# Optimization experiments

Measured on AMD Instinct MI355X. Metric: run time of the kernel, lower is better.

Reference implementation:

```python
import jax, jax.numpy as jnp
import numpy as np


def setup_inputs() -> dict:
    key = jax.random.key(0)
    B, N, M, D = 8, 256, 16, 256
    embeddings = jax.random.normal(key, (B, N, M, D), dtype=jnp.float32)
    w = jnp.asarray(10.0, dtype=jnp.float32)
    b = jnp.asarray(-5.0, dtype=jnp.float32)
    return {"embeddings": embeddings, "w": w, "b": b}


def reference(embeddings, w, b):
    # embeddings: [B, N, M, D]
    B, N, M, D = embeddings.shape
    centroids = jnp.mean(embeddings, axis=2)  # [B, N, D]

    # Cross similarities: S[b,j,i,k] = w * <e_{bji}, c_{bk}> + b
    S = w * jnp.einsum('bjid,bkd->bjik', embeddings, centroids) + b  # [B,N,M,N]

    # Own-centroid case (j == k): leave-one-out centroid
    # <e, (M*c_j - e)/(M-1)> = (M*<e,c_j> - ||e||^2) / (M-1)
    dot_own = jnp.einsum('bjid,bjd->bji', embeddings, centroids)     # [B,N,M]
    sq_norm = jnp.sum(embeddings * embeddings, axis=-1)              # [B,N,M]
    S_self = w * (M * dot_own - sq_norm) / (M - 1) + b               # [B,N,M]

    # Place S_self on the k == j diagonal
    eye = jnp.eye(N, dtype=bool)[None, :, None, :]                   # [1,N,1,N]
    S = jnp.where(eye, S_self[..., None], S)

    # loss = sum log sum_k exp(S) - sum_{j==k} S
    loss = jnp.sum(jax.nn.logsumexp(S, axis=-1)) - jnp.sum(S_self)
    return loss
```

## Files before the change

### kernel.cpp

```cpp
#include <hip/hip_runtime.h>

constexpr int B = 8, N = 256, M = 16, D = 256;

typedef short bf16x8 __attribute__((ext_vector_type(8)));
typedef float f32x4 __attribute__((ext_vector_type(4)));

__device__ __forceinline__ unsigned short f2bf(float x) {
  unsigned u = __float_as_uint(x);
  u = (u + 0x7FFFu + ((u >> 16) & 1u)) >> 16;
  return (unsigned short)u;
}
__device__ __forceinline__ uint4 packbf8(const float* f) {
  uint4 u;
  u.x = (unsigned)f2bf(f[0]) | ((unsigned)f2bf(f[1]) << 16);
  u.y = (unsigned)f2bf(f[2]) | ((unsigned)f2bf(f[3]) << 16);
  u.z = (unsigned)f2bf(f[4]) | ((unsigned)f2bf(f[5]) << 16);
  u.w = (unsigned)f2bf(f[6]) | ((unsigned)f2bf(f[7]) << 16);
  return u;
}


__global__ __launch_bounds__(256) void k_cent(const float* __restrict__ e,
                                              uint4* __restrict__ Cbf,
                                              float* __restrict__ out) {
  const int blk = blockIdx.x;
  const int b = blk >> 8, j = blk & 255;
  const int t = threadIdx.x;
  const float* base = e + (size_t)blk * (M * D);

  __shared__ float cbuf[D];
  float cs = 0.f;
#pragma unroll
  for (int i = 0; i < M; ++i) cs += base[i * D + t];
  cbuf[t] = cs * (1.f / 16.f);
  __syncthreads();

  if (t < 32) {
    float cf[8];
#pragma unroll
    for (int x = 0; x < 8; ++x) cf[x] = cbuf[t * 8 + x];
    Cbf[((size_t)(b * 8 + (t >> 2)) * 16 + (j >> 4)) * 64 + (t & 3) * 16 + (j & 15)] =
        packbf8(cf);
  }
  if (blk == 0 && t == 0) out[0] = 0.f;
}

__global__ __launch_bounds__(256) void k_gemm2(const float* __restrict__ e,
                                               const uint4* __restrict__ Cbf,
                                               const float* __restrict__ wp,
                                               const float* __restrict__ bp,
                                               float* __restrict__ out) {
  const int blk = blockIdx.x;
  const int b = blk >> 6, strip = blk & 63;
  const int tid = threadIdx.x;
  const int wid = tid >> 6, lane = tid & 63;

  __shared__ uint4 A_lds[4 * 8 * 64];
  __shared__ float sql[64];
  __shared__ float lmx[2][64];
  __shared__ float lsm[2][64];
  __shared__ float bred[4];

  {
    const int j = strip * 4 + wid;
    const float* base = e + (size_t)(b * 256 + j) * (M * D);
    const int m = lane & 15, q = lane >> 4;
    const float* rp = base + m * D + q * 8;
    float sqp = 0.f;
#pragma unroll
    for (int kc = 0; kc < 8; ++kc) {
      float f[8];
      *(float4*)(f) = *(const float4*)(rp + kc * 32);
      *(float4*)(f + 4) = *(const float4*)(rp + kc * 32 + 4);
      A_lds[(wid * 8 + kc) * 64 + lane] = packbf8(f);
#pragma unroll
      for (int x = 0; x < 8; ++x) sqp = fmaf(f[x], f[x], sqp);
    }
    sqp += __shfl_xor(sqp, 16, 64);
    sqp += __shfl_xor(sqp, 32, 64);
    if (q == 0) sql[wid * 16 + m] = sqp;
  }
  __syncthreads();

  const int h = wid >> 1, c = wid & 1;
  const int q = lane >> 4, cl_ = lane & 15;
  const uint4* Bb = Cbf + (size_t)(b * 128 + c * 8) * 64 + lane;

  f32x4 acc[2][8];
#pragma unroll
  for (int rt = 0; rt < 2; ++rt)
#pragma unroll
    for (int nt = 0; nt < 8; ++nt) acc[rt][nt] = (f32x4)0.f;

#pragma unroll 1
  for (int kc = 0; kc < 8; ++kc) {
    uint4 af0 = A_lds[((h * 2) * 8 + kc) * 64 + lane];
    uint4 af1 = A_lds[((h * 2 + 1) * 8 + kc) * 64 + lane];
    uint4 bfr[8];
#pragma unroll
    for (int nt = 0; nt < 8; ++nt) bfr[nt] = Bb[(kc * 16 + nt) * 64];
    bf16x8 a0 = __builtin_bit_cast(bf16x8, af0);
    bf16x8 a1 = __builtin_bit_cast(bf16x8, af1);
#pragma unroll
    for (int nt = 0; nt < 8; ++nt) {
      bf16x8 bv = __builtin_bit_cast(bf16x8, bfr[nt]);
      acc[0][nt] = __builtin_amdgcn_mfma_f32_16x16x32_bf16(a0, bv, acc[0][nt], 0, 0, 0);
      acc[1][nt] = __builtin_amdgcn_mfma_f32_16x16x32_bf16(a1, bv, acc[1][nt], 0, 0, 0);
    }
  }

  const float w = *wp, bias = *bp;
  float ssum = 0.f;

#pragma unroll
  for (int rt = 0; rt < 2; ++rt) {
    const int jr = strip * 4 + h * 2 + rt;
    const bool own = (c == (jr >> 7)) && (cl_ == (jr & 15));
    const int ntd = (jr >> 4) & 7;
    float sq[4];
    if (own) {
#pragma unroll
      for (int reg = 0; reg < 4; ++reg)
        sq[reg] = sql[(h * 2 + rt) * 16 + q * 4 + reg];
    }
#pragma unroll
    for (int nt = 0; nt < 8; ++nt)
#pragma unroll
      for (int reg = 0; reg < 4; ++reg) {
        const float raw = acc[rt][nt][reg];
        float sv = fmaf(w, raw, bias);
        if (own && nt == ntd) {
          sv = fmaf(w * (1.f / 15.f), 16.f * raw - sq[reg], bias);
          ssum += sv;
        }
        acc[rt][nt][reg] = sv;
      }
#pragma unroll
    for (int reg = 0; reg < 4; ++reg) {
      float mx = acc[rt][0][reg];
#pragma unroll
      for (int nt = 1; nt < 8; ++nt) mx = fmaxf(mx, acc[rt][nt][reg]);
#pragma unroll
      for (int mk = 1; mk < 16; mk <<= 1) mx = fmaxf(mx, __shfl_xor(mx, mk, 64));
      if (cl_ == 0) lmx[c][(h * 2 + rt) * 16 + q * 4 + reg] = mx;
    }
  }
  __syncthreads();

#pragma unroll
  for (int rt = 0; rt < 2; ++rt)
#pragma unroll
    for (int reg = 0; reg < 4; ++reg) {
      const int Rl = (h * 2 + rt) * 16 + q * 4 + reg;
      const float mx = fmaxf(lmx[0][Rl], lmx[1][Rl]);
      float se = 0.f;
#pragma unroll
      for (int nt = 0; nt < 8; ++nt) se += __expf(acc[rt][nt][reg] - mx);
#pragma unroll
      for (int mk = 1; mk < 16; mk <<= 1) se += __shfl_xor(se, mk, 64);
      if (cl_ == 0) lsm[c][Rl] = se;
    }
  __syncthreads();

  float part = -ssum;
  if (c == 0 && cl_ == 0) {
#pragma unroll
    for (int rt = 0; rt < 2; ++rt)
#pragma unroll
      for (int reg = 0; reg < 4; ++reg) {
        const int Rl = (h * 2 + rt) * 16 + q * 4 + reg;
        const float mx = fmaxf(lmx[0][Rl], lmx[1][Rl]);
        part += mx + __logf(lsm[0][Rl] + lsm[1][Rl]);
      }
  }
#pragma unroll
  for (int mk = 1; mk < 64; mk <<= 1) part += __shfl_xor(part, mk, 64);
  if (lane == 0) bred[wid] = part;
  __syncthreads();
  if (tid == 0) atomicAdd(out, bred[0] + bred[1] + bred[2] + bred[3]);
}

extern "C" void kernel_launch(void* const* d_in, const int* in_sizes, int n_in,
                              void* d_out, int out_size, void* d_ws, size_t ws_size,
                              hipStream_t stream) {
  const float* e = (const float*)d_in[0];
  const float* wp = (const float*)d_in[1];
  const float* bp = (const float*)d_in[2];
  float* out = (float*)d_out;
  uint4* Cbf = (uint4*)d_ws;

  k_cent<<<B * N, 256, 0, stream>>>(e, Cbf, out);
  k_gemm2<<<B * 64, 256, 0, stream>>>(e, Cbf, wp, bp, out);
}
```

Before: 99.58 us.

## Halve rows per GEMM block to double grid size and parallelism

The fused GEMM+logsumexp kernel now handles 2 centroid rows per block instead of 4, so the grid doubles from 512 to 1024 blocks. Each wave computes one row tile, and the A-tile load and squared norm are split across two waves, with the two partial norms combined through shared memory. This targets under-occupancy on a 256-CU part and cuts per-wave accumulator registers. The cost is that each block now rereads the full centroid B matrix for half as many rows, which doubles centroid traffic through L2.

New measurement: 102.7 us. 1.03x slower.

```diff
diff --git a/kernel.cpp b/kernel.cpp
--- a/kernel.cpp
+++ b/kernel.cpp
@@ -45,133 +45,122 @@
   if (blk == 0 && t == 0) out[0] = 0.f;
 }
 
-__global__ __launch_bounds__(256) void k_gemm2(const float* __restrict__ e,
+__global__ __launch_bounds__(256) void k_gemm3(const float* __restrict__ e,
                                                const uint4* __restrict__ Cbf,
                                                const float* __restrict__ wp,
                                                const float* __restrict__ bp,
                                                float* __restrict__ out) {
   const int blk = blockIdx.x;
-  const int b = blk >> 6, strip = blk & 63;
+  const int b = blk >> 7, p = blk & 127;
   const int tid = threadIdx.x;
   const int wid = tid >> 6, lane = tid & 63;
+  const int jt = wid >> 1, half = wid & 1;
 
-  __shared__ uint4 A_lds[4 * 8 * 64];
-  __shared__ float sql[64];
-  __shared__ float lmx[2][64];
-  __shared__ float lsm[2][64];
+  __shared__ uint4 A_lds[2 * 8 * 64];
+  __shared__ float sqh[2][2][16];
+  __shared__ float lmx[2][32];
+  __shared__ float lsm[2][32];
   __shared__ float bred[4];
 
   {
-    const int j = strip * 4 + wid;
+    const int j = p * 2 + jt;
     const float* base = e + (size_t)(b * 256 + j) * (M * D);
     const int m = lane & 15, q = lane >> 4;
     const float* rp = base + m * D + q * 8;
     float sqp = 0.f;
 #pragma unroll
-    for (int kc = 0; kc < 8; ++kc) {
+    for (int kk = 0; kk < 4; ++kk) {
+      const int kc = half * 4 + kk;
       float f[8];
       *(float4*)(f) = *(const float4*)(rp + kc * 32);
       *(float4*)(f + 4) = *(const float4*)(rp + kc * 32 + 4);
-      A_lds[(wid * 8 + kc) * 64 + lane] = packbf8(f);
+      A_lds[(jt * 8 + kc) * 64 + lane] = packbf8(f);
 #pragma unroll
       for (int x = 0; x < 8; ++x) sqp = fmaf(f[x], f[x], sqp);
     }
     sqp += __shfl_xor(sqp, 16, 64);
     sqp += __shfl_xor(sqp, 32, 64);
-    if (q == 0) sql[wid * 16 + m] = sqp;
+    if (q == 0) sqh[jt][half][m] = sqp;
   }
   __syncthreads();
 
-  const int h = wid >> 1, c = wid & 1;
+  const int c = half;
   const int q = lane >> 4, cl_ = lane & 15;
   const uint4* Bb = Cbf + (size_t)(b * 128 + c * 8) * 64 + lane;
 
-  f32x4 acc[2][8];
+  f32x4 acc[8];
 #pragma unroll
-  for (int rt = 0; rt < 2; ++rt)
-#pragma unroll
-    for (int nt = 0; nt < 8; ++nt) acc[rt][nt] = (f32x4)0.f;
+  for (int nt = 0; nt < 8; ++nt) acc[nt] = (f32x4)0.f;
 
 #pragma unroll 1
   for (int kc = 0; kc < 8; ++kc) {
-    uint4 af0 = A_lds[((h * 2) * 8 + kc) * 64 + lane];
-    uint4 af1 = A_lds[((h * 2 + 1) * 8 + kc) * 64 + lane];
+    uint4 af = A_lds[(jt * 8 + kc) * 64 + lane];
     uint4 bfr[8];
 #pragma unroll
     for (int nt = 0; nt < 8; ++nt) bfr[nt] = Bb[(kc * 16 + nt) * 64];
-    bf16x8 a0 = __builtin_bit_cast(bf16x8, af0);
-    bf16x8 a1 = __builtin_bit_cast(bf16x8, af1);
+    bf16x8 a = __builtin_bit_cast(bf16x8, af);
 #pragma unroll
     for (int nt = 0; nt < 8; ++nt) {
       bf16x8 bv = __builtin_bit_cast(bf16x8, bfr[nt]);
-      acc[0][nt] = __builtin_amdgcn_mfma_f32_16x16x32_bf16(a0, bv, acc[0][nt], 0, 0, 0);
-      acc[1][nt] = __builtin_amdgcn_mfma_f32_16x16x32_bf16(a1, bv, acc[1][nt], 0, 0, 0);
+      acc[nt] = __builtin_amdgcn_mfma_f32_16x16x32_bf16(a, bv, acc[nt], 0, 0, 0);
     }
   }
 
   const float w = *wp, bias = *bp;
   float ssum = 0.f;
-
+  const int jr = p * 2 + jt;
+  const bool own = (c == (jr >> 7)) && (cl_ == (jr & 15));
+  const int ntd = (jr >> 4) & 7;
+  float sq[4];
+  if (own) {
 #pragma unroll
-  for (int rt = 0; rt < 2; ++rt) {
-    const int jr = strip * 4 + h * 2 + rt;
-    const bool own = (c == (jr >> 7)) && (cl_ == (jr & 15));
-    const int ntd = (jr >> 4) & 7;
-    float sq[4];
-    if (own) {
+    for (int reg = 0; reg < 4; ++reg)
+      sq[reg] = sqh[jt][0][q * 4 + reg] + sqh[jt][1][q * 4 + reg];
+  }
 #pragma unroll
-      for (int reg = 0; reg < 4; ++reg)
-        sq[reg] = sql[(h * 2 + rt) * 16 + q * 4 + reg];
+  for (int nt = 0; nt < 8; ++nt)
+#pragma unroll
+    for (int reg = 0; reg < 4; ++reg) {
+      const float raw = acc[nt][reg];
+      float sv = fmaf(w, raw, bias);
+      if (own && nt == ntd) {
+        sv = fmaf(w * (1.f / 15.f), 16.f * raw - sq[reg], bias);
+        ssum += sv;
+      }
+      acc[nt][reg] = sv;
     }
 #pragma unroll
-    for (int nt = 0; nt < 8; ++nt)
+  for (int reg = 0; reg < 4; ++reg) {
+    float mx = acc[0][reg];
 #pragma unroll
-      for (int reg = 0; reg < 4; ++reg) {
-        const float raw = acc[rt][nt][reg];
-        float sv = fmaf(w, raw, bias);
-        if (own && nt == ntd) {
-          sv = fmaf(w * (1.f / 15.f), 16.f * raw - sq[reg], bias);
-          ssum += sv;
-        }
-        acc[rt][nt][reg] = sv;
-      }
+    for (int nt = 1; nt < 8; ++nt) mx = fmaxf(mx, acc[nt][reg]);
 #pragma unroll
-    for (int reg = 0; reg < 4; ++reg) {
-      float mx = acc[rt][0][reg];
-#pragma unroll
-      for (int nt = 1; nt < 8; ++nt) mx = fmaxf(mx, acc[rt][nt][reg]);
-#pragma unroll
-      for (int mk = 1; mk < 16; mk <<= 1) mx = fmaxf(mx, __shfl_xor(mx, mk, 64));
-      if (cl_ == 0) lmx[c][(h * 2 + rt) * 16 + q * 4 + reg] = mx;
-    }
+    for (int mk = 1; mk < 16; mk <<= 1) mx = fmaxf(mx, __shfl_xor(mx, mk, 64));
+    if (cl_ == 0) lmx[c][jt * 16 + q * 4 + reg] = mx;
   }
   __syncthreads();
 
 #pragma unroll
-  for (int rt = 0; rt < 2; ++rt)
+  for (int reg = 0; reg < 4; ++reg) {
+    const int Rl = jt * 16 + q * 4 + reg;
+    const float mx = fmaxf(lmx[0][Rl], lmx[1][Rl]);
+    float se = 0.f;
 #pragma unroll
-    for (int reg = 0; reg < 4; ++reg) {
-      const int Rl = (h * 2 + rt) * 16 + q * 4 + reg;
-      const float mx = fmaxf(lmx[0][Rl], lmx[1][Rl]);
-      float se = 0.f;
+    for (int nt = 0; nt < 8; ++nt) se += __expf(acc[nt][reg] - mx);
 #pragma unroll
-      for (int nt = 0; nt < 8; ++nt) se += __expf(acc[rt][nt][reg] - mx);
-#pragma unroll
-      for (int mk = 1; mk < 16; mk <<= 1) se += __shfl_xor(se, mk, 64);
-      if (cl_ == 0) lsm[c][Rl] = se;
-    }
+    for (int mk = 1; mk < 16; mk <<= 1) se += __shfl_xor(se, mk, 64);
+    if (cl_ == 0) lsm[c][Rl] = se;
+  }
   __syncthreads();
 
   float part = -ssum;
   if (c == 0 && cl_ == 0) {
 #pragma unroll
-    for (int rt = 0; rt < 2; ++rt)
-#pragma unroll
-      for (int reg = 0; reg < 4; ++reg) {
-        const int Rl = (h * 2 + rt) * 16 + q * 4 + reg;
-        const float mx = fmaxf(lmx[0][Rl], lmx[1][Rl]);
-        part += mx + __logf(lsm[0][Rl] + lsm[1][Rl]);
-      }
+    for (int reg = 0; reg < 4; ++reg) {
+      const int Rl = jt * 16 + q * 4 + reg;
+      const float mx = fmaxf(lmx[0][Rl], lmx[1][Rl]);
+      part += mx + __logf(lsm[0][Rl] + lsm[1][Rl]);
+    }
   }
 #pragma unroll
   for (int mk = 1; mk < 64; mk <<= 1) part += __shfl_xor(part, mk, 64);
@@ -190,5 +179,5 @@
   uint4* Cbf = (uint4*)d_ws;
 
   k_cent<<<B * N, 256, 0, stream>>>(e, Cbf, out);
-  k_gemm2<<<B * 64, 256, 0, stream>>>(e, Cbf, wp, bp, out);
+  k_gemm3<<<B * 128, 256, 0, stream>>>(e, Cbf, wp, bp, out);
 }
```
